# Performance work log

Hardware: AMD Instinct MI355X
Metric: run time of the kernel (lower is better)

## Reference

```python
import jax, jax.numpy as jnp
import numpy as np

# Static config matching init_kwargs / input_specs
IN_CH = 256
PATCH = 64
LAYERS = 4
B, H, W = 4, 256, 256
IC = IN_CH // 4        # SelfAttention inner channels (reduce=4)
C16 = IN_CH // 16      # f_test conv output channels
ALPHA = 0.05


def conv1x1(x, w, b):
    # x: (b,c,h,w), w: (out,c), b: (out,)  == nn.Conv2d(c,out,1)
    return jnp.einsum('bchw,oc->bohw', x, w) + b[None, :, None, None]


def setup_inputs() -> dict:
    key = jax.random.key(0)
    ks = jax.random.split(key, 12)
    s = 0.05
    return {
        'x':  jax.random.normal(ks[0], (B, IN_CH, H, W), jnp.float32),
        'Wq': jax.random.normal(ks[1], (IC, IN_CH), jnp.float32) * s,
        'bq': jax.random.normal(ks[2], (IC,), jnp.float32) * s,
        'Wk': jax.random.normal(ks[3], (IC, IN_CH), jnp.float32) * s,
        'bk': jax.random.normal(ks[4], (IC,), jnp.float32) * s,
        'Wv': jax.random.normal(ks[5], (IC, IN_CH), jnp.float32) * s,
        'bv': jax.random.normal(ks[6], (IC,), jnp.float32) * s,
        'Wr': jax.random.normal(ks[7], (IN_CH, IC), jnp.float32) * s,
        'br': jax.random.normal(ks[8], (IN_CH,), jnp.float32) * s,
        'Wf': jax.random.normal(ks[9], (C16, IN_CH), jnp.float32) * s,
        'bf': jax.random.normal(ks[10], (C16,), jnp.float32) * s,
    }


def reference(x, Wq, bq, Wk, bk, Wv, bv, Wr, br, Wf, bf):
    b, c, h, w = x.shape
    p = PATCH
    nh = h // p
    ic = IC

    # f_test applies the same 1x1 conv to the FULL image every call; its output
    # is identical each time, so precompute the per-(batch,channel) mean/var once.
    # torch uses .detach() -> stop_gradient.
    y2 = jax.lax.stop_gradient(conv1x1(x, Wf, bf))           # (b, C16, h, w)
    m2 = y2.mean(axis=(2, 3))                                 # (b, C16)
    v2 = y2.var(axis=(2, 3))                                  # biased var
    n1 = float(p * p)
    n2 = float(h * w)
    dfw = n1 + n2 - 2.0

    def ftest_decision(patch):
        # Two-group one-way ANOVA (scipy.stats.f_oneway) per (batch, channel).
        y1 = jax.lax.stop_gradient(conv1x1(patch, Wf, bf))    # (b, C16, p, p)
        m1 = y1.mean(axis=(2, 3))
        v1 = y1.var(axis=(2, 3))
        gm = (n1 * m1 + n2 * m2) / (n1 + n2)
        ssb = n1 * (m1 - gm) ** 2 + n2 * (m2 - gm) ** 2       # df_between = 1
        ssw = n1 * v1 + n2 * v2                               # sum sq dev within
        Fst = ssb / (ssw / dfw)
        # p-value = sf of F(1, dfw) = I_{dfw/(dfw+F)}(dfw/2, 1/2)
        pval = jax.scipy.special.betainc(dfw / 2.0, 0.5, dfw / (dfw + Fst))
        counts = jnp.sum(pval < ALPHA)
        return counts * 2 >= m1.size                          # scalar bool

    def attn(patch):
        # SelfAttention.forward: channel-to-channel attention over a patch.
        Q = conv1x1(patch, Wq, bq).reshape(b, ic, p * p)      # (b, ic, pp)
        # NOTE: original does K_pro.view(b, -1, inner_ch) -- a raw reshape,
        # NOT a transpose; we reproduce that exactly.
        K = conv1x1(patch, Wk, bk).reshape(b, p * p, ic)      # (b, pp, ic)
        V = conv1x1(patch, Wv, bv).reshape(b, ic, p * p)
        wts = jax.nn.softmax(jnp.einsum('bim,bmj->bij', Q, K), axis=1)  # (b,ic,ic)
        att = jnp.einsum('bij,bjm->bim', wts, V).reshape(b, ic, p, p)
        return conv1x1(att, Wr, br) + patch

    def run_patch(patch):
        # layer loop with data-dependent early break, expressed via masking
        stopped = jnp.array(False)
        for _ in range(LAYERS):
            stopped = stopped | ftest_decision(patch)  # break BEFORE attention
            patch = jnp.where(stopped, patch, attn(patch))
        return patch

    # Extract all nh*nh patches: (n_patches, b, c, p, p)
    patches = (x.reshape(b, c, nh, p, nh, p)
                .transpose(2, 4, 0, 1, 3, 5)
                .reshape(nh * nh, b, c, p, p))
    out_patches = jax.vmap(run_patch)(patches)

    # Faithful to original bug: x1 = x.clone() happens inside the patch loop,
    # so only the LAST patch's update survives in the returned tensor.
    x1 = x.at[:, :, (nh - 1) * p:, (nh - 1) * p:].set(out_patches[-1])
    return x1
```

## Files before the change

kernel.cpp:

```cpp
#include <hip/hip_runtime.h>

#define FCRIT 3.8415923532

#define OFF_FULL   0u
#define OFF_PATCH  1024u
#define OFF_S      8192u
#define OFF_Y3     1048576u
#define STATS_ZERO_BYTES 270336u

static __device__ __forceinline__ double wred(double v) {
#pragma unroll
  for (int off = 32; off > 0; off >>= 1) v += __shfl_down(v, off, 64);
  return v;
}

static __device__ __forceinline__ bool is_stopped(const double* __restrict__ fullS,
                                                  const double* __restrict__ patchS,
                                                  int upto) {
  const int k = threadIdx.x & 63;
  const double fs = fullS[2 * k], fq = fullS[2 * k + 1];
  const double m2 = fs * (1.0 / 65536.0);
  const double v2 = fq * (1.0 / 65536.0) - m2 * m2;
  bool stopped = false;
  for (int l = 0; l <= upto; ++l) {
    const double* ps = patchS + (size_t)l * 128;
    const double s1 = ps[2 * k], s2 = ps[2 * k + 1];
    const double m1 = s1 * (1.0 / 4096.0);
    const double v1 = s2 * (1.0 / 4096.0) - m1 * m1;
    const double gm = (4096.0 * m1 + 65536.0 * m2) * (1.0 / 69632.0);
    const double d1 = m1 - gm, d2 = m2 - gm;
    const double ssb = 4096.0 * d1 * d1 + 65536.0 * d2 * d2;
    const double ssw = 4096.0 * v1 + 65536.0 * v2;
    const double F = ssb * (69630.0 / ssw);
    const unsigned long long bal = __ballot(F > FCRIT);
    const int cnt = __popcll(bal);
    stopped = stopped || (2 * cnt >= 64);
  }
  return stopped;
}

static __device__ __forceinline__ void fma16(float acc[4][4], float4 w, float4 v) {
  const float wa[4] = {w.x, w.y, w.z, w.w};
  const float va[4] = {v.x, v.y, v.z, v.w};
#pragma unroll
  for (int a = 0; a < 4; ++a)
#pragma unroll
    for (int c = 0; c < 4; ++c) acc[a][c] += wa[a] * va[c];
}

static __device__ __forceinline__ size_t pidx(int b, int c, int y, int x) {
  return (((size_t)b * 256 + c) * 256 + 192 + y) * 256 + 192 + x;
}

__global__ __launch_bounds__(256) void k_main(const float* __restrict__ x,
                                              const float* __restrict__ Wf,
                                              const float* __restrict__ bf,
                                              float* __restrict__ out,
                                              double* __restrict__ fullS,
                                              double* __restrict__ patchS0) {
  __shared__ __align__(16) float WfT2[16 * 257];
  __shared__ __align__(16) float WfT[256 * 16];
  __shared__ double sm[4][16][2];
  __shared__ double sp[4][16][2];
  const int t = threadIdx.x;
  const int bb = blockIdx.x >> 7;
  const int rp = blockIdx.x & 127;

  for (int r = 0; r < 16; ++r) {
    int idx = r * 256 + t;
    WfT2[(idx >> 8) * 257 + (idx & 255)] = Wf[idx];
  }
  __syncthreads();
  for (int r = 0; r < 16; ++r) {
    int idx = r * 256 + t;
    int c = idx >> 4, o = idx & 15;
    WfT[c * 16 + o] = WfT2[o * 257 + c];
  }
  __syncthreads();

  const int r0 = rp * 2 + (t >> 7);
  const int col2 = (t & 127) * 2;
  const size_t base = (size_t)bb * 16777216 + (size_t)r0 * 256 + col2;
  const float* xp = x + base;
  float* op = out + base;
  const bool pStore = (rp >= 96) && ((t & 127) >= 96);

  float y0[16], y1[16];
#pragma unroll
  for (int o = 0; o < 16; ++o) { y0[o] = 0.f; y1[o] = 0.f; }

  for (int cb = 0; cb < 32; ++cb) {
    double v[8];
#pragma unroll
    for (int u = 0; u < 8; ++u)
      v[u] = *reinterpret_cast<const double*>(xp + (size_t)(cb * 8 + u) * 65536);
#pragma unroll
    for (int u = 0; u < 8; ++u) {
      double* dst = reinterpret_cast<double*>(op + (size_t)(cb * 8 + u) * 65536);
      if (pStore) *dst = v[u];
      else __builtin_nontemporal_store(v[u], dst);
      const int c = cb * 8 + u;
      float2 f = *reinterpret_cast<const float2*>(&v[u]);
      const float4* wf = reinterpret_cast<const float4*>(&WfT[c * 16]);
      const float4 w0 = wf[0], w1 = wf[1], w2 = wf[2], w3 = wf[3];
      const float wv[16] = {w0.x, w0.y, w0.z, w0.w, w1.x, w1.y, w1.z, w1.w,
                            w2.x, w2.y, w2.z, w2.w, w3.x, w3.y, w3.z, w3.w};
#pragma unroll
      for (int o = 0; o < 16; ++o) {
        y0[o] += wv[o] * f.x;
        y1[o] += wv[o] * f.y;
      }
    }
  }

  const int w = t >> 6, lane = t & 63;
  const bool pBlock = (rp >= 96);
  const bool pLane = ((t & 127) >= 96);
#pragma unroll 1
  for (int o = 0; o < 16; ++o) {
    const float bo = bf[o];
    const double a0 = (double)(y0[o] + bo), a1 = (double)(y1[o] + bo);
    double s1 = a0 + a1, s2 = a0 * a0 + a1 * a1;
    const double r1 = wred(s1), r2 = wred(s2);
    if (lane == 0) { sm[w][o][0] = r1; sm[w][o][1] = r2; }
    if (pBlock) {
      double p1 = pLane ? s1 : 0.0, p2 = pLane ? s2 : 0.0;
      p1 = wred(p1); p2 = wred(p2);
      if (lane == 0) { sp[w][o][0] = p1; sp[w][o][1] = p2; }
    }
  }
  __syncthreads();
  if (t < 32) {
    const int o = t >> 1, wh = t & 1;
    double s = sm[0][o][wh] + sm[1][o][wh] + sm[2][o][wh] + sm[3][o][wh];
    unsafeAtomicAdd(&fullS[(bb * 16 + o) * 2 + wh], s);
    if (pBlock) {
      double p = sp[0][o][wh] + sp[1][o][wh] + sp[2][o][wh] + sp[3][o][wh];
      unsafeAtomicAdd(&patchS0[(bb * 16 + o) * 2 + wh], p);
    }
  }
}

__global__ __launch_bounds__(256) void k_qkv(const float* __restrict__ out,
                                             const float* __restrict__ Wq, const float* __restrict__ bq,
                                             const float* __restrict__ Wk, const float* __restrict__ bk,
                                             const float* __restrict__ Wv, const float* __restrict__ bv,
                                             float* __restrict__ Y3,
                                             const double* __restrict__ fullS,
                                             const double* __restrict__ patchS, int layer) {
  if (is_stopped(fullS, patchS, layer)) return;
  __shared__ __align__(16) float W3T[64][68];
  __shared__ __align__(16) float X2[64 * 64];
  const int t = threadIdx.x;
  const int blk = blockIdx.x;
  const int qt = blk & 63;
  const int mt = (blk >> 6) % 3;
  const int bb = blk / 192;
  const float* Wm = (mt == 0) ? Wq : (mt == 1) ? Wk : Wv;
  const float* bm = (mt == 0) ? bq : (mt == 1) ? bk : bv;
  const int tq = t & 15, to = t >> 4;
  float acc[4][4] = {};
  for (int kc = 0; kc < 4; ++kc) {
    const int k0 = kc * 64;
    __syncthreads();
    for (int r = 0; r < 16; ++r) {
      int idx = r * 256 + t;
      int ml = idx >> 6, kl = idx & 63;
      W3T[kl][ml] = Wm[ml * 256 + k0 + kl];
    }
    for (int r = 0; r < 16; ++r) {
      int idx = r * 256 + t;
      int kl = idx >> 6, ql = idx & 63;
      X2[kl * 64 + ql] = out[pidx(bb, k0 + kl, qt, ql)];
    }
    __syncthreads();
#pragma unroll 8
    for (int kk = 0; kk < 64; ++kk) {
      const float4 wv = *reinterpret_cast<const float4*>(&W3T[kk][to * 4]);
      const float4 xv = *reinterpret_cast<const float4*>(&X2[kk * 64 + tq * 4]);
      fma16(acc, wv, xv);
    }
  }
#pragma unroll
  for (int a = 0; a < 4; ++a) {
    const int ml = to * 4 + a;
    const float bias = bm[ml];
    float4 res;
    res.x = acc[a][0] + bias;
    res.y = acc[a][1] + bias;
    res.z = acc[a][2] + bias;
    res.w = acc[a][3] + bias;
    *reinterpret_cast<float4*>(&Y3[((size_t)bb * 192 + mt * 64 + ml) * 4096 + qt * 64 + tq * 4]) = res;
  }
}

__global__ __launch_bounds__(256) void k_s(const float* __restrict__ Y3,
                                           float* __restrict__ Sbase,
                                           const double* __restrict__ fullS,
                                           const double* __restrict__ patchS, int layer) {
  if (is_stopped(fullS, patchS, layer)) return;
  __shared__ __align__(16) float QT[64][68];
  __shared__ __align__(16) float K2[64 * 64];
  const int t = threadIdx.x;
  const int mc = blockIdx.x & 63;
  const int bb = blockIdx.x >> 6;
  const int m0 = mc * 64;
  const float* Q = Y3 + (size_t)bb * 192 * 4096;
  const float* Kf = Q + 64 * 4096;
  for (int r = 0; r < 16; ++r) {
    int idx = r * 256 + t;
    int i = idx >> 6, ml = idx & 63;
    QT[ml][i] = Q[(size_t)i * 4096 + m0 + ml];
  }
  for (int r = 0; r < 16; ++r) {
    int idx = r * 256 + t;
    K2[idx] = Kf[(size_t)m0 * 64 + idx];
  }
  __syncthreads();
  const int tj = t & 15, ti = t >> 4;
  float acc[4][4] = {};
#pragma unroll 8
  for (int mm = 0; mm < 64; ++mm) {
    const float4 qv = *reinterpret_cast<const float4*>(&QT[mm][ti * 4]);
    const float4 kv = *reinterpret_cast<const float4*>(&K2[mm * 64 + tj * 4]);
    fma16(acc, qv, kv);
  }
  float* Sl = Sbase + (size_t)layer * 16384 + bb * 4096;
#pragma unroll
  for (int a = 0; a < 4; ++a)
#pragma unroll
    for (int c = 0; c < 4; ++c)
      unsafeAtomicAdd(&Sl[(ti * 4 + a) * 64 + tj * 4 + c], acc[a][c]);
}

__global__ __launch_bounds__(256) void k_awr(const float* __restrict__ Y3,
                                             const float* __restrict__ Sbase,
                                             const float* __restrict__ Wr,
                                             const float* __restrict__ br,
                                             float* __restrict__ out,
                                             const double* __restrict__ fullS,
                                             const double* __restrict__ patchS, int layer) {
  if (is_stopped(fullS, patchS, layer)) return;
  __shared__ __align__(16) float Sw[64 * 68];
  __shared__ __align__(16) float AV[64 * 68];
  __shared__ __align__(16) float WrF[128 * 65];
  const int t = threadIdx.x;
  const int y = blockIdx.x & 63;
  const int oh = (blockIdx.x >> 6) & 1;
  const int bb = blockIdx.x >> 7;

  const float* Vp = Y3 + (size_t)bb * 192 * 4096 + (size_t)128 * 4096 + y * 64;
  for (int r = 0; r < 16; ++r) {
    int idx = r * 256 + t;
    int j = idx >> 6, xx = idx & 63;
    AV[j * 68 + xx] = Vp[(size_t)j * 4096 + xx];
  }
  const float* Sl = Sbase + (size_t)layer * 16384 + bb * 4096;
  for (int r = 0; r < 16; ++r) {
    int idx = r * 256 + t;
    Sw[(idx & 63) * 68 + (idx >> 6)] = Sl[idx];
  }
  for (int r = 0; r < 32; ++r) {
    int idx = r * 256 + t;
    int ol = idx >> 6, i = idx & 63;
    WrF[ol * 65 + i] = Wr[(oh * 128 + ol) * 64 + i];
  }
  __syncthreads();

  if (t < 64) {
    float* colp = &Sw[t * 68];
    float mx = -1e30f;
#pragma unroll
    for (int i = 0; i < 64; ++i) mx = fmaxf(mx, colp[i]);
    float sum = 0.f;
#pragma unroll
    for (int i = 0; i < 64; ++i) {
      float e = __expf(colp[i] - mx);
      colp[i] = e;
      sum += e;
    }
    const float inv = 1.f / sum;
#pragma unroll
    for (int i = 0; i < 64; ++i) colp[i] *= inv;
  }
  __syncthreads();

  {
    const int ti = t >> 4, tx = t & 15;
    float acc[4][4] = {};
#pragma unroll 8
    for (int j = 0; j < 64; ++j) {
      const float4 wv = *reinterpret_cast<const float4*>(&Sw[j * 68 + ti * 4]);
      const float4 vv = *reinterpret_cast<const float4*>(&AV[j * 68 + tx * 4]);
      fma16(acc, wv, vv);
    }
    __syncthreads();
#pragma unroll
    for (int a = 0; a < 4; ++a) {
      float4 res;
      res.x = acc[a][0]; res.y = acc[a][1]; res.z = acc[a][2]; res.w = acc[a][3];
      *reinterpret_cast<float4*>(&AV[(ti * 4 + a) * 68 + tx * 4]) = res;
    }
  }
  __syncthreads();

  const int to = t >> 3, tx8 = t & 7;
  float acc[4][8] = {};
#pragma unroll 4
  for (int i = 0; i < 64; ++i) {
    const float4 a0 = *reinterpret_cast<const float4*>(&AV[i * 68 + tx8 * 8]);
    const float4 a1 = *reinterpret_cast<const float4*>(&AV[i * 68 + tx8 * 8 + 4]);
    const float av[8] = {a0.x, a0.y, a0.z, a0.w, a1.x, a1.y, a1.z, a1.w};
#pragma unroll
    for (int a = 0; a < 4; ++a) {
      const float wv = WrF[(to * 4 + a) * 65 + i];
#pragma unroll
      for (int c = 0; c < 8; ++c) acc[a][c] += wv * av[c];
    }
  }
#pragma unroll
  for (int a = 0; a < 4; ++a) {
    const int o = oh * 128 + to * 4 + a;
    const float bro = br[o];
    float* p = out + pidx(bb, o, y, tx8 * 8);
    float4 p0 = *reinterpret_cast<const float4*>(p);
    float4 p1 = *reinterpret_cast<const float4*>(p + 4);
    p0.x += acc[a][0] + bro; p0.y += acc[a][1] + bro;
    p0.z += acc[a][2] + bro; p0.w += acc[a][3] + bro;
    p1.x += acc[a][4] + bro; p1.y += acc[a][5] + bro;
    p1.z += acc[a][6] + bro; p1.w += acc[a][7] + bro;
    *reinterpret_cast<float4*>(p) = p0;
    *reinterpret_cast<float4*>(p + 4) = p1;
  }
}

__global__ __launch_bounds__(256) void k_ftest(const float* __restrict__ out,
                                               const float* __restrict__ Wf,
                                               const float* __restrict__ bf,
                                               double* __restrict__ patchS,
                                               const double* __restrict__ fullS, int layer) {
  if (is_stopped(fullS, patchS, layer)) return;
  __shared__ __align__(16) float WfT2[16 * 257];
  __shared__ __align__(16) float WfT[256 * 16];
  __shared__ float part[2 * 128 * 17];
  __shared__ double red[16][16][2];
  const int t = threadIdx.x;
  const int bb = blockIdx.x >> 5;
  const int rg = blockIdx.x & 31;

  for (int r = 0; r < 16; ++r) {
    int idx = r * 256 + t;
    WfT2[(idx >> 8) * 257 + (idx & 255)] = Wf[idx];
  }
  __syncthreads();
  for (int r = 0; r < 16; ++r) {
    int idx = r * 256 + t;
    int c = idx >> 4, o = idx & 15;
    WfT[c * 16 + o] = WfT2[o * 257 + c];
  }
  __syncthreads();

  const int h = t >> 7;
  const int px = t & 127;
  const int row = 192 + rg * 2 + (px >> 6);
  const int col = 192 + (px & 63);
  const size_t base = (size_t)bb * 16777216 + (size_t)h * 128 * 65536 + (size_t)row * 256 + col;

  float y[16] = {};
  for (int cb = 0; cb < 16; ++cb) {
    float v[8];
#pragma unroll
    for (int u = 0; u < 8; ++u)
      v[u] = out[base + (size_t)(cb * 8 + u) * 65536];
#pragma unroll
    for (int u = 0; u < 8; ++u) {
      const int c = h * 128 + cb * 8 + u;
      const float4* wf = reinterpret_cast<const float4*>(&WfT[c * 16]);
      const float4 w0 = wf[0], w1 = wf[1], w2 = wf[2], w3 = wf[3];
      const float wv[16] = {w0.x, w0.y, w0.z, w0.w, w1.x, w1.y, w1.z, w1.w,
                            w2.x, w2.y, w2.z, w2.w, w3.x, w3.y, w3.z, w3.w};
#pragma unroll
      for (int o = 0; o < 16; ++o) y[o] += wv[o] * v[u];
    }
  }
#pragma unroll
  for (int o = 0; o < 16; ++o) part[(h * 128 + px) * 17 + o] = y[o];
  __syncthreads();

  const int oo = t & 15, pxg = t >> 4;
  double s1 = 0.0, s2 = 0.0;
  const float bo = bf[oo];
#pragma unroll
  for (int j = 0; j < 8; ++j) {
    const int p = pxg * 8 + j;
    const float yv = part[p * 17 + oo] + part[(128 + p) * 17 + oo] + bo;
    const double v = (double)yv;
    s1 += v;
    s2 += v * v;
  }
  red[oo][pxg][0] = s1;
  red[oo][pxg][1] = s2;
  __syncthreads();
  if (t < 32) {
    const int o = t >> 1, wh = t & 1;
    double s = 0.0;
#pragma unroll
    for (int g = 0; g < 16; ++g) s += red[o][g][wh];
    unsafeAtomicAdd(&patchS[(size_t)(layer + 1) * 128 + (bb * 16 + o) * 2 + wh], s);
  }
}

extern "C" void kernel_launch(void* const* d_in, const int* in_sizes, int n_in,
                              void* d_out, int out_size, void* d_ws, size_t ws_size,
                              hipStream_t stream) {
  const float* x  = (const float*)d_in[0];
  const float* Wq = (const float*)d_in[1];
  const float* bq = (const float*)d_in[2];
  const float* Wk = (const float*)d_in[3];
  const float* bk = (const float*)d_in[4];
  const float* Wv = (const float*)d_in[5];
  const float* bv = (const float*)d_in[6];
  const float* Wr = (const float*)d_in[7];
  const float* br = (const float*)d_in[8];
  const float* Wf = (const float*)d_in[9];
  const float* bf = (const float*)d_in[10];
  float* out = (float*)d_out;
  char* ws = (char*)d_ws;

  double* fullS  = (double*)(ws + OFF_FULL);
  double* patchS = (double*)(ws + OFF_PATCH);
  float* Sb = (float*)(ws + OFF_S);
  float* Y3 = (float*)(ws + OFF_Y3);

  (void)hipMemsetAsync(ws, 0, STATS_ZERO_BYTES, stream);
  k_main<<<512, 256, 0, stream>>>(x, Wf, bf, out, fullS, patchS);
  for (int l = 0; l < 4; ++l) {
    k_qkv<<<768, 256, 0, stream>>>(out, Wq, bq, Wk, bk, Wv, bv, Y3, fullS, patchS, l);
    k_s<<<256, 256, 0, stream>>>(Y3, Sb, fullS, patchS, l);
    k_awr<<<512, 256, 0, stream>>>(Y3, Sb, Wr, br, out, fullS, patchS, l);
    if (l < 3) k_ftest<<<128, 256, 0, stream>>>(out, Wf, bf, patchS, fullS, l);
  }
}
```

Baseline: 260.7 us.

## Fuse pipeline into persistent megakernel with split-bf16 MFMA and grid barriers

Replaces the per-layer launch chain (qkv, S, awr, ftest) with one persistent kernel. 192 blocks stream the full-image copy and statistics while 64 blocks process the patch layers, synchronising through global atomic barriers. Patch matmuls use bf16 MFMA with hi/mid/lo weight and hi/mid activation splits to approximate fp32 accuracy, and a small kernel pre-converts the weights. The aim is to remove launch overhead, overlap the bandwidth-bound copy with patch compute, and use matrix cores. The risks are spin-barrier deadlock or timeout if the blocks are not co-resident, and some loss of precision.

```diff
diff --git a/kernel.cpp b/kernel.cpp
--- a/kernel.cpp
+++ b/kernel.cpp
@@ -1,412 +1,621 @@
 #include <hip/hip_runtime.h>
+
+typedef __attribute__((ext_vector_type(8))) short short8;
+typedef __attribute__((ext_vector_type(8))) unsigned short us8;
+typedef __attribute__((ext_vector_type(4))) unsigned short us4;
+typedef __attribute__((ext_vector_type(4))) float f32x4;
 
 #define FCRIT 3.8415923532
 
 #define OFF_FULL   0u
 #define OFF_PATCH  1024u
-#define OFF_S      8192u
-#define OFF_Y3     1048576u
-#define STATS_ZERO_BYTES 270336u
-
+#define OFF_SBUF   8192u
+#define OFF_BAR    270336u
+#define ZERO_BYTES 270592u
+#define OFF_W3H    (1u<<20)
+#define OFF_WRH    (OFF_W3H + 294912u)
+#define OFF_WFH    (OFF_WRH + 98304u)
+#define OFF_QBT    (4u<<20)
+#define OFF_KB     (8u<<20)
+#define OFF_VBT    (12u<<20)
+#define OFF_XB     (16u<<20)
+#define OFF_PB     (32u<<20)
+
+static __device__ __forceinline__ unsigned short f2bf(float f) {
+  union { float f; unsigned u; } v; v.f = f;
+  unsigned r = v.u + 0x7fffu + ((v.u >> 16) & 1u);
+  return (unsigned short)(r >> 16);
+}
+static __device__ __forceinline__ float bf2f(unsigned short h) {
+  union { unsigned u; float f; } v; v.u = ((unsigned)h) << 16;
+  return v.f;
+}
+static __device__ __forceinline__ void split2(float v, unsigned short& h, unsigned short& m) {
+  h = f2bf(v); float r = v - bf2f(h); m = f2bf(r);
+}
 static __device__ __forceinline__ double wred(double v) {
 #pragma unroll
   for (int off = 32; off > 0; off >>= 1) v += __shfl_down(v, off, 64);
   return v;
 }
-
-static __device__ __forceinline__ bool is_stopped(const double* __restrict__ fullS,
-                                                  const double* __restrict__ patchS,
-                                                  int upto) {
-  const int k = threadIdx.x & 63;
-  const double fs = fullS[2 * k], fq = fullS[2 * k + 1];
-  const double m2 = fs * (1.0 / 65536.0);
-  const double v2 = fq * (1.0 / 65536.0) - m2 * m2;
-  bool stopped = false;
-  for (int l = 0; l <= upto; ++l) {
-    const double* ps = patchS + (size_t)l * 128;
-    const double s1 = ps[2 * k], s2 = ps[2 * k + 1];
-    const double m1 = s1 * (1.0 / 4096.0);
-    const double v1 = s2 * (1.0 / 4096.0) - m1 * m1;
-    const double gm = (4096.0 * m1 + 65536.0 * m2) * (1.0 / 69632.0);
-    const double d1 = m1 - gm, d2 = m2 - gm;
-    const double ssb = 4096.0 * d1 * d1 + 65536.0 * d2 * d2;
-    const double ssw = 4096.0 * v1 + 65536.0 * v2;
-    const double F = ssb * (69630.0 / ssw);
-    const unsigned long long bal = __ballot(F > FCRIT);
-    const int cnt = __popcll(bal);
-    stopped = stopped || (2 * cnt >= 64);
-  }
-  return stopped;
-}
-
-static __device__ __forceinline__ void fma16(float acc[4][4], float4 w, float4 v) {
-  const float wa[4] = {w.x, w.y, w.z, w.w};
-  const float va[4] = {v.x, v.y, v.z, v.w};
-#pragma unroll
-  for (int a = 0; a < 4; ++a)
-#pragma unroll
-    for (int c = 0; c < 4; ++c) acc[a][c] += wa[a] * va[c];
-}
-
-static __device__ __forceinline__ size_t pidx(int b, int c, int y, int x) {
-  return (((size_t)b * 256 + c) * 256 + 192 + y) * 256 + 192 + x;
-}
-
-__global__ __launch_bounds__(256) void k_main(const float* __restrict__ x,
-                                              const float* __restrict__ Wf,
-                                              const float* __restrict__ bf,
-                                              float* __restrict__ out,
-                                              double* __restrict__ fullS,
-                                              double* __restrict__ patchS0) {
-  __shared__ __align__(16) float WfT2[16 * 257];
-  __shared__ __align__(16) float WfT[256 * 16];
-  __shared__ double sm[4][16][2];
-  __shared__ double sp[4][16][2];
-  const int t = threadIdx.x;
-  const int bb = blockIdx.x >> 7;
-  const int rp = blockIdx.x & 127;
-
-  for (int r = 0; r < 16; ++r) {
-    int idx = r * 256 + t;
-    WfT2[(idx >> 8) * 257 + (idx & 255)] = Wf[idx];
+static __device__ __forceinline__ void gbar(unsigned* cnt, unsigned target) {
+  __syncthreads();
+  if (threadIdx.x == 0) {
+    __threadfence();
+    atomicAdd(cnt, 1u);
+    unsigned spins = 0;
+    while (__hip_atomic_load(cnt, __ATOMIC_RELAXED, __HIP_MEMORY_SCOPE_AGENT) < target) {
+      __builtin_amdgcn_s_sleep(2);
+      if (++spins > (1u << 20)) break;
+    }
+    __threadfence();
   }
   __syncthreads();
-  for (int r = 0; r < 16; ++r) {
-    int idx = r * 256 + t;
-    int c = idx >> 4, o = idx & 15;
-    WfT[c * 16 + o] = WfT2[o * 257 + c];
+}
+
+__global__ __launch_bounds__(256) void k_wcvt(const float* __restrict__ Wq,
+                                              const float* __restrict__ Wk,
+                                              const float* __restrict__ Wv,
+                                              const float* __restrict__ Wr,
+                                              const float* __restrict__ Wf,
+                                              char* __restrict__ ws) {
+  unsigned short* W3H = (unsigned short*)(ws + OFF_W3H);
+  unsigned short* WRH = (unsigned short*)(ws + OFF_WRH);
+  unsigned short* WFH = (unsigned short*)(ws + OFF_WFH);
+  for (int i = blockIdx.x * 256 + threadIdx.x; i < 69632; i += gridDim.x * 256) {
+    float v; unsigned short* dst; int stride;
+    if (i < 49152) {
+      const int row = i >> 8, col = i & 255;
+      v = (row < 64) ? Wq[row * 256 + col]
+        : (row < 128) ? Wk[(row - 64) * 256 + col]
+                      : Wv[(row - 128) * 256 + col];
+      dst = W3H + i; stride = 49152;
+    } else if (i < 65536) {
+      v = Wr[i - 49152]; dst = WRH + (i - 49152); stride = 16384;
+    } else {
+      v = Wf[i - 65536]; dst = WFH + (i - 65536); stride = 4096;
+    }
+    const unsigned short h = f2bf(v); const float r1 = v - bf2f(h);
+    const unsigned short m = f2bf(r1); const float r2 = r1 - bf2f(m);
+    dst[0] = h; dst[stride] = m; dst[2 * stride] = f2bf(r2);
   }
-  __syncthreads();
-
-  const int r0 = rp * 2 + (t >> 7);
-  const int col2 = (t & 127) * 2;
-  const size_t base = (size_t)bb * 16777216 + (size_t)r0 * 256 + col2;
-  const float* xp = x + base;
-  float* op = out + base;
-  const bool pStore = (rp >= 96) && ((t & 127) >= 96);
-
-  float y0[16], y1[16];
-#pragma unroll
-  for (int o = 0; o < 16; ++o) { y0[o] = 0.f; y1[o] = 0.f; }
-
-  for (int cb = 0; cb < 32; ++cb) {
-    double v[8];
-#pragma unroll
-    for (int u = 0; u < 8; ++u)
-      v[u] = *reinterpret_cast<const double*>(xp + (size_t)(cb * 8 + u) * 65536);
-#pragma unroll
-    for (int u = 0; u < 8; ++u) {
-      double* dst = reinterpret_cast<double*>(op + (size_t)(cb * 8 + u) * 65536);
-      if (pStore) *dst = v[u];
-      else __builtin_nontemporal_store(v[u], dst);
-      const int c = cb * 8 + u;
-      float2 f = *reinterpret_cast<const float2*>(&v[u]);
-      const float4* wf = reinterpret_cast<const float4*>(&WfT[c * 16]);
-      const float4 w0 = wf[0], w1 = wf[1], w2 = wf[2], w3 = wf[3];
-      const float wv[16] = {w0.x, w0.y, w0.z, w0.w, w1.x, w1.y, w1.z, w1.w,
-                            w2.x, w2.y, w2.z, w2.w, w3.x, w3.y, w3.z, w3.w};
-#pragma unroll
-      for (int o = 0; o < 16; ++o) {
-        y0[o] += wv[o] * f.x;
-        y1[o] += wv[o] * f.y;
-      }
-    }
-  }
-
+}
+
+__global__ __launch_bounds__(256, 1) void k_mega(
+    const float* __restrict__ x, const float* __restrict__ bq,
+    const float* __restrict__ bk, const float* __restrict__ bv,
+    const float* __restrict__ br, const float* __restrict__ bf,
+    const float* __restrict__ Wf, float* __restrict__ out,
+    char* __restrict__ ws) {
+  __shared__ __align__(16) char pool[55296];
+  const int t = threadIdx.x;
+  const int bid = blockIdx.x;
+  double* fullS  = (double*)(ws + OFF_FULL);
+  double* patchS = (double*)(ws + OFF_PATCH);
+  float* Sb = (float*)(ws + OFF_SBUF);
+  unsigned* cntA = (unsigned*)(ws + OFF_BAR);
+  unsigned* cntG = (unsigned*)(ws + OFF_BAR + 128);
+  unsigned short* W3H = (unsigned short*)(ws + OFF_W3H);
+  unsigned short* WRH = (unsigned short*)(ws + OFF_WRH);
+  unsigned short* WFH = (unsigned short*)(ws + OFF_WFH);
+  unsigned short* QBT = (unsigned short*)(ws + OFF_QBT);
+  unsigned short* KB  = (unsigned short*)(ws + OFF_KB);
+  unsigned short* VBT = (unsigned short*)(ws + OFF_VBT);
+  unsigned short* XB  = (unsigned short*)(ws + OFF_XB);
+  float* PB = (float*)(ws + OFF_PB);
   const int w = t >> 6, lane = t & 63;
-  const bool pBlock = (rp >= 96);
-  const bool pLane = ((t & 127) >= 96);
-#pragma unroll 1
-  for (int o = 0; o < 16; ++o) {
-    const float bo = bf[o];
-    const double a0 = (double)(y0[o] + bo), a1 = (double)(y1[o] + bo);
-    double s1 = a0 + a1, s2 = a0 * a0 + a1 * a1;
-    const double r1 = wred(s1), r2 = wred(s2);
-    if (lane == 0) { sm[w][o][0] = r1; sm[w][o][1] = r2; }
-    if (pBlock) {
-      double p1 = pLane ? s1 : 0.0, p2 = pLane ? s2 : 0.0;
-      p1 = wred(p1); p2 = wred(p2);
-      if (lane == 0) { sp[w][o][0] = p1; sp[w][o][1] = p2; }
-    }
-  }
-  __syncthreads();
-  if (t < 32) {
-    const int o = t >> 1, wh = t & 1;
-    double s = sm[0][o][wh] + sm[1][o][wh] + sm[2][o][wh] + sm[3][o][wh];
-    unsafeAtomicAdd(&fullS[(bb * 16 + o) * 2 + wh], s);
-    if (pBlock) {
-      double p = sp[0][o][wh] + sp[1][o][wh] + sp[2][o][wh] + sp[3][o][wh];
-      unsafeAtomicAdd(&patchS0[(bb * 16 + o) * 2 + wh], p);
-    }
-  }
-}
-
-__global__ __launch_bounds__(256) void k_qkv(const float* __restrict__ out,
-                                             const float* __restrict__ Wq, const float* __restrict__ bq,
-                                             const float* __restrict__ Wk, const float* __restrict__ bk,
-                                             const float* __restrict__ Wv, const float* __restrict__ bv,
-                                             float* __restrict__ Y3,
-                                             const double* __restrict__ fullS,
-                                             const double* __restrict__ patchS, int layer) {
-  if (is_stopped(fullS, patchS, layer)) return;
-  __shared__ __align__(16) float W3T[64][68];
-  __shared__ __align__(16) float X2[64 * 64];
-  const int t = threadIdx.x;
-  const int blk = blockIdx.x;
-  const int qt = blk & 63;
-  const int mt = (blk >> 6) % 3;
-  const int bb = blk / 192;
-  const float* Wm = (mt == 0) ? Wq : (mt == 1) ? Wk : Wv;
-  const float* bm = (mt == 0) ? bq : (mt == 1) ? bk : bv;
-  const int tq = t & 15, to = t >> 4;
-  float acc[4][4] = {};
-  for (int kc = 0; kc < 4; ++kc) {
-    const int k0 = kc * 64;
+  const int lo16 = lane & 15, hi4 = lane >> 4;
+
+  if (bid < 192) {
+    float* WfT2 = (float*)pool;
+    float* WfT  = (float*)(pool + 16448);
+    double* sm  = (double*)(pool + 32896);
+    for (int r = 0; r < 16; ++r) {
+      int idx = r * 256 + t;
+      WfT2[(idx >> 8) * 257 + (idx & 255)] = Wf[idx];
+    }
     __syncthreads();
     for (int r = 0; r < 16; ++r) {
       int idx = r * 256 + t;
-      int ml = idx >> 6, kl = idx & 63;
-      W3T[kl][ml] = Wm[ml * 256 + k0 + kl];
-    }
-    for (int r = 0; r < 16; ++r) {
-      int idx = r * 256 + t;
-      int kl = idx >> 6, ql = idx & 63;
-      X2[kl * 64 + ql] = out[pidx(bb, k0 + kl, qt, ql)];
+      int c = idx >> 4, o = idx & 15;
+      WfT[c * 16 + o] = WfT2[o * 257 + c];
     }
     __syncthreads();
-#pragma unroll 8
-    for (int kk = 0; kk < 64; ++kk) {
-      const float4 wv = *reinterpret_cast<const float4*>(&W3T[kk][to * 4]);
-      const float4 xv = *reinterpret_cast<const float4*>(&X2[kk * 64 + tq * 4]);
-      fma16(acc, wv, xv);
+    for (int rp = bid; rp < 512; rp += 192) {
+      const int bb = rp >> 7;
+      const int r0 = (rp & 127) * 2 + (t >> 7);
+      const int col2 = (t & 127) * 2;
+      const size_t base = (size_t)bb * 16777216 + (size_t)r0 * 256 + col2;
+      const float* xp = x + base;
+      float* op = out + base;
+      float y0[16], y1[16];
+#pragma unroll
+      for (int o = 0; o < 16; ++o) { y0[o] = 0.f; y1[o] = 0.f; }
+      for (int cb = 0; cb < 32; ++cb) {
+        double v[8];
+#pragma unroll
+        for (int u = 0; u < 8; ++u)
+          v[u] = *reinterpret_cast<const double*>(xp + (size_t)(cb * 8 + u) * 65536);
+#pragma unroll
+        for (int u = 0; u < 8; ++u) {
+          __builtin_nontemporal_store(v[u], reinterpret_cast<double*>(op + (size_t)(cb * 8 + u) * 65536));
+          const int c = cb * 8 + u;
+          float2 f = *reinterpret_cast<const float2*>(&v[u]);
+          const float4* wf = reinterpret_cast<const float4*>(&WfT[c * 16]);
+          const float4 w0 = wf[0], w1 = wf[1], w2 = wf[2], w3 = wf[3];
+          const float wv[16] = {w0.x, w0.y, w0.z, w0.w, w1.x, w1.y, w1.z, w1.w,
+                                w2.x, w2.y, w2.z, w2.w, w3.x, w3.y, w3.z, w3.w};
+#pragma unroll
+          for (int o = 0; o < 16; ++o) {
+            y0[o] += wv[o] * f.x;
+            y1[o] += wv[o] * f.y;
+          }
+        }
+      }
+#pragma unroll 1
+      for (int o = 0; o < 16; ++o) {
+        const float bo = bf[o];
+        const double a0 = (double)(y0[o] + bo), a1 = (double)(y1[o] + bo);
+        double s1 = a0 + a1, s2 = a0 * a0 + a1 * a1;
+        const double r1 = wred(s1), r2 = wred(s2);
+        if (lane == 0) { sm[(w * 16 + o) * 2] = r1; sm[(w * 16 + o) * 2 + 1] = r2; }
+      }
+      __syncthreads();
+      if (t < 32) {
+        const int o = t >> 1, wh = t & 1;
+        double s = sm[o * 2 + wh] + sm[(16 + o) * 2 + wh] + sm[(32 + o) * 2 + wh] + sm[(48 + o) * 2 + wh];
+        unsafeAtomicAdd(&fullS[(bb * 16 + o) * 2 + wh], s);
+      }
+      __syncthreads();
+    }
+  } else {
+    const int bid2 = bid - 192;
+    const int b = bid2 >> 4;
+    const int q16 = bid2 & 15;
+    unsigned barSeq = 0;
+    for (int layer = 0; layer < 4; ++layer) {
+      const float* Pprev = PB + (size_t)(layer - 1) * 4194304;
+      const int px0 = q16 * 256;
+      {
+        unsigned short* XhL = (unsigned short*)pool;
+        unsigned short* XmL = (unsigned short*)(pool + 20480);
+        const int pxg = px0 + t;
+        f32x4 fa[4];
+#pragma unroll
+        for (int nf = 0; nf < 4; ++nf) fa[nf] = (f32x4)0.f;
+        for (int kc = 0; kc < 8; ++kc) {
+          const int c0 = kc * 32;
+          __syncthreads();
+          float vv[32];
+          if (layer == 0) {
+            const float* xp = x + (size_t)b * 16777216 + (size_t)(192 + (pxg >> 6)) * 256
+                              + (192 + (pxg & 63)) + (size_t)c0 * 65536;
+#pragma unroll
+            for (int u = 0; u < 32; ++u) vv[u] = xp[(size_t)u * 65536];
+          } else {
+            const float* pp = Pprev + ((size_t)b * 4096 + pxg) * 256 + c0;
+#pragma unroll
+            for (int u = 0; u < 8; ++u)
+              *reinterpret_cast<float4*>(&vv[u * 4]) = reinterpret_cast<const float4*>(pp)[u];
+          }
+          unsigned short* xh = XB + ((size_t)b * 4096 + pxg) * 256 + c0;
+#pragma unroll
+          for (int g = 0; g < 4; ++g) {
+            us8 hv, mv;
+#pragma unroll
+            for (int j = 0; j < 8; ++j) {
+              unsigned short h, m; split2(vv[g * 8 + j], h, m);
+              hv[j] = h; mv[j] = m;
+            }
+            *(us8*)&XhL[t * 40 + g * 8] = hv;
+            *(us8*)&XmL[t * 40 + g * 8] = mv;
+            *(us8*)(xh + g * 8) = hv;
+            *(us8*)(xh + 4194304 + g * 8) = mv;
+          }
+          __syncthreads();
+          const short8 ah = *(const short8*)(WFH + lo16 * 256 + c0 + hi4 * 8);
+          const short8 am = *(const short8*)(WFH + 4096 + lo16 * 256 + c0 + hi4 * 8);
+          const short8 al = *(const short8*)(WFH + 8192 + lo16 * 256 + c0 + hi4 * 8);
+#pragma unroll
+          for (int nf = 0; nf < 4; ++nf) {
+            const int pxl = w * 64 + nf * 16 + lo16;
+            const short8 bh = *(const short8*)&XhL[pxl * 40 + hi4 * 8];
+            const short8 bm = *(const short8*)&XmL[pxl * 40 + hi4 * 8];
+            f32x4 c = fa[nf];
+            c = __builtin_amdgcn_mfma_f32_16x16x32_bf16(ah, bh, c, 0, 0, 0);
+            c = __builtin_amdgcn_mfma_f32_16x16x32_bf16(ah, bm, c, 0, 0, 0);
+            c = __builtin_amdgcn_mfma_f32_16x16x32_bf16(am, bh, c, 0, 0, 0);
+            c = __builtin_amdgcn_mfma_f32_16x16x32_bf16(am, bm, c, 0, 0, 0);
+            c = __builtin_amdgcn_mfma_f32_16x16x32_bf16(al, bh, c, 0, 0, 0);
+            fa[nf] = c;
+          }
+        }
+#pragma unroll
+        for (int r = 0; r < 4; ++r) {
+          const int o = hi4 * 4 + r;
+          const float bo = bf[o];
+          double s1 = 0.0, s2 = 0.0;
+#pragma unroll
+          for (int nf = 0; nf < 4; ++nf) {
+            const double v = (double)(fa[nf][r] + bo);
+            s1 += v; s2 += v * v;
+          }
+#pragma unroll
+          for (int msk = 1; msk < 16; msk <<= 1) {
+            s1 += __shfl_xor(s1, msk, 64);
+            s2 += __shfl_xor(s2, msk, 64);
+          }
+          if (lo16 == 0) {
+            unsafeAtomicAdd(&patchS[layer * 128 + (b * 16 + o) * 2], s1);
+            unsafeAtomicAdd(&patchS[layer * 128 + (b * 16 + o) * 2 + 1], s2);
+          }
+        }
+      }
+      gbar(cntA, 64 * (++barSeq));
+      {
+        unsigned short* WhL = (unsigned short*)pool;
+        unsigned short* XhB = (unsigned short*)(pool + 30720);
+        const unsigned short* W3L2 = W3H + 2 * 49152;
+        for (int ph = 0; ph < 2; ++ph) {
+          f32x4 bacc[12][2];
+#pragma unroll
+          for (int mf = 0; mf < 12; ++mf)
+#pragma unroll
+            for (int nf = 0; nf < 2; ++nf) bacc[mf][nf] = (f32x4)0.f;
+          for (int kc = 0; kc < 8; ++kc) {
+            const int c0 = kc * 32;
+            __syncthreads();
+#pragma unroll
+            for (int lev = 0; lev < 2; ++lev) {
+#pragma unroll
+              for (int r = 0; r < 3; ++r) {
+                const int unit = r * 256 + t;
+                const int m = unit >> 2, k8 = (unit & 3) * 8;
+                *(us8*)&WhL[lev * 7680 + m * 40 + k8] =
+                    *(const us8*)(W3H + lev * 49152 + m * 256 + c0 + k8);
+              }
+#pragma unroll
+              for (int r = 0; r < 2; ++r) {
+                const int unit = r * 256 + t;
+                const int px = unit >> 2, k8 = (unit & 3) * 8;
+                *(us8*)&XhB[lev * 5120 + px * 40 + k8] =
+                    *(const us8*)(XB + (size_t)lev * 4194304
+                                  + ((size_t)b * 4096 + px0 + ph * 128 + px) * 256 + c0 + k8);
+              }
+            }
+            __syncthreads();
+            short8 xbh[2], xbm[2];
+#pragma unroll
+            for (int nf = 0; nf < 2; ++nf) {
+              const int pxl = w * 32 + nf * 16 + lo16;
+              xbh[nf] = *(const short8*)&XhB[pxl * 40 + hi4 * 8];
+              xbm[nf] = *(const short8*)&XhB[5120 + pxl * 40 + hi4 * 8];
+            }
+#pragma unroll
+            for (int mf = 0; mf < 12; ++mf) {
+              const int m = mf * 16 + lo16;
+              const short8 wh = *(const short8*)&WhL[m * 40 + hi4 * 8];
+              const short8 wm = *(const short8*)&WhL[7680 + m * 40 + hi4 * 8];
+              const short8 wl = *(const short8*)(W3L2 + m * 256 + c0 + hi4 * 8);
+#pragma unroll
+              for (int nf = 0; nf < 2; ++nf) {
+                f32x4 c = bacc[mf][nf];
+                c = __builtin_amdgcn_mfma_f32_16x16x32_bf16(wh, xbh[nf], c, 0, 0, 0);
+                c = __builtin_amdgcn_mfma_f32_16x16x32_bf16(wh, xbm[nf], c, 0, 0, 0);
+                c = __builtin_amdgcn_mfma_f32_16x16x32_bf16(wm, xbh[nf], c, 0, 0, 0);
+                c = __builtin_amdgcn_mfma_f32_16x16x32_bf16(wm, xbm[nf], c, 0, 0, 0);
+                c = __builtin_amdgcn_mfma_f32_16x16x32_bf16(wl, xbh[nf], c, 0, 0, 0);
+                bacc[mf][nf] = c;
+              }
+            }
+          }
+#pragma unroll
+          for (int mf = 0; mf < 12; ++mf) {
+            const int m0 = mf * 16 + hi4 * 4;
+            const float* bias = (m0 < 64) ? bq + m0 : (m0 < 128) ? bk + (m0 - 64) : bv + (m0 - 128);
+#pragma unroll
+            for (int nf = 0; nf < 2; ++nf) {
+              const int pxg = px0 + ph * 128 + w * 32 + nf * 16 + lo16;
+              us4 hv, mv;
+#pragma unroll
+              for (int r = 0; r < 4; ++r) {
+                unsigned short h, m;
+                split2(bacc[mf][nf][r] + bias[r], h, m);
+                hv[r] = h; mv[r] = m;
+              }
+              if (mf < 4) {
+                const size_t o = ((size_t)b * 4096 + pxg) * 64 + m0;
+                *(us4*)(QBT + o) = hv;
+                *(us4*)(QBT + 1048576 + o) = mv;
+              } else if (mf < 8) {
+#pragma unroll
+                for (int r = 0; r < 4; ++r) {
+                  const size_t o = ((size_t)b * 64 + (m0 - 64 + r)) * 4096 + pxg;
+                  KB[o] = hv[r];
+                  KB[1048576 + o] = mv[r];
+                }
+              } else {
+                const size_t o = ((size_t)b * 4096 + pxg) * 64 + (m0 - 128);
+                *(us4*)(VBT + o) = hv;
+                *(us4*)(VBT + 1048576 + o) = mv;
+              }
+            }
+          }
+        }
+      }
+      gbar(cntA, 64 * (++barSeq));
+      {
+        unsigned short* At = (unsigned short*)pool;
+        unsigned short* Bt = (unsigned short*)(pool + 18432);
+        f32x4 cacc[4];
+#pragma unroll
+        for (int mf = 0; mf < 4; ++mf) cacc[mf] = (f32x4)0.f;
+        for (int mcl = 0; mcl < 4; ++mcl) {
+          const int mc = q16 * 4 + mcl;
+          __syncthreads();
+          {
+            const int r2 = t >> 2, ig = (t & 3) * 16;
+#pragma unroll
+            for (int lev = 0; lev < 2; ++lev) {
+              const size_t qb = (size_t)lev * 1048576 + ((size_t)b * 4096 + mc * 64 + r2) * 64 + ig;
+              const us8 v0 = *(const us8*)(QBT + qb);
+              const us8 v1 = *(const us8*)(QBT + qb + 8);
+#pragma unroll
+              for (int ii = 0; ii < 8; ++ii) {
+                At[lev * 4608 + (ig + ii) * 72 + r2] = v0[ii];
+                At[lev * 4608 + (ig + 8 + ii) * 72 + r2] = v1[ii];
+              }
+            }
+            const int p0 = t * 16;
+            const int jj0 = p0 & 63, rr = p0 >> 6;
+#pragma unroll
+            for (int lev = 0; lev < 2; ++lev) {
+              const size_t kb = (size_t)lev * 1048576 + ((size_t)b * 64 + mc) * 4096 + p0;
+              const us8 v0 = *(const us8*)(KB + kb);
+              const us8 v1 = *(const us8*)(KB + kb + 8);
+#pragma unroll
+              for (int ii = 0; ii < 8; ++ii) {
+                Bt[lev * 4608 + (jj0 + ii) * 72 + rr] = v0[ii];
+                Bt[lev * 4608 + (jj0 + 8 + ii) * 72 + rr] = v1[ii];
+              }
+            }
+          }
+          __syncthreads();
+#pragma unroll
+          for (int kc = 0; kc < 2; ++kc) {
+            const short8 bh = *(const short8*)&Bt[(w * 16 + lo16) * 72 + kc * 32 + hi4 * 8];
+            const short8 bm = *(const short8*)&Bt[4608 + (w * 16 + lo16) * 72 + kc * 32 + hi4 * 8];
+#pragma unroll
+            for (int mf = 0; mf < 4; ++mf) {
+              const short8 qh = *(const short8*)&At[(mf * 16 + lo16) * 72 + kc * 32 + hi4 * 8];
+              const short8 qm = *(const short8*)&At[4608 + (mf * 16 + lo16) * 72 + kc * 32 + hi4 * 8];
+              f32x4 c = cacc[mf];
+              c = __builtin_amdgcn_mfma_f32_16x16x32_bf16(qh, bh, c, 0, 0, 0);
+              c = __builtin_amdgcn_mfma_f32_16x16x32_bf16(qh, bm, c, 0, 0, 0);
+              c = __builtin_amdgcn_mfma_f32_16x16x32_bf16(qm, bh, c, 0, 0, 0);
+              c = __builtin_amdgcn_mfma_f32_16x16x32_bf16(qm, bm, c, 0, 0, 0);
+              cacc[mf] = c;
+            }
+          }
+        }
+        float* Sl = Sb + ((size_t)layer * 4 + b) * 4096;
+#pragma unroll
+        for (int mf = 0; mf < 4; ++mf)
+#pragma unroll
+          for (int r = 0; r < 4; ++r)
+            unsafeAtomicAdd(&Sl[(mf * 16 + hi4 * 4 + r) * 64 + w * 16 + lo16], cacc[mf][r]);
+      }
+      gbar(cntA, 64 * (++barSeq));
+      {
+        unsigned short* wtsL = (unsigned short*)pool;
+        unsigned short* AbT  = (unsigned short*)(pool + 18432);
+        float* Sf = (float*)(pool + 18432);
+        const float* Sl = Sb + ((size_t)layer * 4 + b) * 4096;
+        {
+          const int i2 = t >> 2, jg = (t & 3) * 16;
+#pragma unroll
+          for (int u = 0; u < 4; ++u) {
+            const float4 v = *(const float4*)(Sl + i2 * 64 + jg + u * 4);
+            Sf[(jg + u * 4 + 0) * 68 + i2] = v.x;
+            Sf[(jg + u * 4 + 1) * 68 + i2] = v.y;
+            Sf[(jg + u * 4 + 2) * 68 + i2] = v.z;
+            Sf[(jg + u * 4 + 3) * 68 + i2] = v.w;
+          }
+        }
+        __syncthreads();
+        if (t < 64) {
+          float* rowp = &Sf[t * 68];
+          float mx = -1e30f;
+#pragma unroll
+          for (int i = 0; i < 64; ++i) mx = fmaxf(mx, rowp[i]);
+          float sum = 0.f;
+#pragma unroll
+          for (int i = 0; i < 64; ++i) {
+            const float e = __expf(rowp[i] - mx);
+            rowp[i] = e; sum += e;
+          }
+          const float inv = 1.f / sum;
+#pragma unroll
+          for (int i = 0; i < 64; ++i) rowp[i] *= inv;
+        }
+        __syncthreads();
+        {
+          const int i2 = t >> 2, jg = (t & 3) * 16;
+#pragma unroll
+          for (int u = 0; u < 2; ++u) {
+            us8 hv, mv;
+#pragma unroll
+            for (int jj = 0; jj < 8; ++jj) {
+              unsigned short h, m;
+              split2(Sf[(jg + u * 8 + jj) * 68 + i2], h, m);
+              hv[jj] = h; mv[jj] = m;
+            }
+            *(us8*)&wtsL[i2 * 72 + jg + u * 8] = hv;
+            *(us8*)&wtsL[4608 + i2 * 72 + jg + u * 8] = mv;
+          }
+        }
+        __syncthreads();
+        float* PBl = PB + (size_t)layer * 4194304;
+        for (int ph = 0; ph < 2; ++ph) {
+          f32x4 a1[4][2];
+#pragma unroll
+          for (int mf = 0; mf < 4; ++mf)
+#pragma unroll
+            for (int nf = 0; nf < 2; ++nf) a1[mf][nf] = (f32x4)0.f;
+#pragma unroll
+          for (int kc = 0; kc < 2; ++kc) {
+            short8 vh[2], vm[2];
+#pragma unroll
+            for (int nf = 0; nf < 2; ++nf) {
+              const int pxg = px0 + ph * 128 + w * 32 + nf * 16 + lo16;
+              const size_t vb = ((size_t)b * 4096 + pxg) * 64 + kc * 32 + hi4 * 8;
+              vh[nf] = *(const short8*)(VBT + vb);
+              vm[nf] = *(const short8*)(VBT + 1048576 + vb);
+            }
+#pragma unroll
+            for (int mf = 0; mf < 4; ++mf) {
+              const short8 wh = *(const short8*)&wtsL[(mf * 16 + lo16) * 72 + kc * 32 + hi4 * 8];
+              const short8 wm = *(const short8*)&wtsL[4608 + (mf * 16 + lo16) * 72 + kc * 32 + hi4 * 8];
+#pragma unroll
+              for (int nf = 0; nf < 2; ++nf) {
+                f32x4 c = a1[mf][nf];
+                c = __builtin_amdgcn_mfma_f32_16x16x32_bf16(wh, vh[nf], c, 0, 0, 0);
+                c = __builtin_amdgcn_mfma_f32_16x16x32_bf16(wh, vm[nf], c, 0, 0, 0);
+                c = __builtin_amdgcn_mfma_f32_16x16x32_bf16(wm, vh[nf], c, 0, 0, 0);
+                c = __builtin_amdgcn_mfma_f32_16x16x32_bf16(wm, vm[nf], c, 0, 0, 0);
+                a1[mf][nf] = c;
+              }
+            }
+          }
+#pragma unroll
+          for (int mf = 0; mf < 4; ++mf)
+#pragma unroll
+            for (int nf = 0; nf < 2; ++nf) {
+              const int pxl = w * 32 + nf * 16 + lo16;
+              const int i0 = mf * 16 + hi4 * 4;
+              us4 hv, mv;
+#pragma unroll
+              for (int r = 0; r < 4; ++r) {
+                unsigned short h, m;
+                split2(a1[mf][nf][r], h, m);
+                hv[r] = h; mv[r] = m;
+              }
+              *(us4*)&AbT[pxl * 72 + i0] = hv;
+              *(us4*)&AbT[9216 + pxl * 72 + i0] = mv;
+            }
+          __syncthreads();
+          f32x4 a2[16][2];
+#pragma unroll
+          for (int mf = 0; mf < 16; ++mf)
+#pragma unroll
+            for (int nf = 0; nf < 2; ++nf) a2[mf][nf] = (f32x4)0.f;
+#pragma unroll
+          for (int kc = 0; kc < 2; ++kc) {
+            short8 abh[2], abm[2];
+#pragma unroll
+            for (int nf = 0; nf < 2; ++nf) {
+              const int pxl = w * 32 + nf * 16 + lo16;
+              abh[nf] = *(const short8*)&AbT[pxl * 72 + kc * 32 + hi4 * 8];
+              abm[nf] = *(const short8*)&AbT[9216 + pxl * 72 + kc * 32 + hi4 * 8];
+            }
+#pragma unroll
+            for (int mf = 0; mf < 16; ++mf) {
+              const int o = mf * 16 + lo16;
+              const short8 rh = *(const short8*)(WRH + o * 64 + kc * 32 + hi4 * 8);
+              const short8 rm = *(const short8*)(WRH + 16384 + o * 64 + kc * 32 + hi4 * 8);
+              const short8 rl = *(const short8*)(WRH + 32768 + o * 64 + kc * 32 + hi4 * 8);
+#pragma unroll
+              for (int nf = 0; nf < 2; ++nf) {
+                f32x4 c = a2[mf][nf];
+                c = __builtin_amdgcn_mfma_f32_16x16x32_bf16(rh, abh[nf], c, 0, 0, 0);
+                c = __builtin_amdgcn_mfma_f32_16x16x32_bf16(rh, abm[nf], c, 0, 0, 0);
+                c = __builtin_amdgcn_mfma_f32_16x16x32_bf16(rm, abh[nf], c, 0, 0, 0);
+                c = __builtin_amdgcn_mfma_f32_16x16x32_bf16(rm, abm[nf], c, 0, 0, 0);
+                c = __builtin_amdgcn_mfma_f32_16x16x32_bf16(rl, abh[nf], c, 0, 0, 0);
+                a2[mf][nf] = c;
+              }
+            }
+          }
+#pragma unroll
+          for (int mf = 0; mf < 16; ++mf) {
+#pragma unroll
+            for (int nf = 0; nf < 2; ++nf) {
+              const int pxg = px0 + ph * 128 + w * 32 + nf * 16 + lo16;
+              const int o0 = mf * 16 + hi4 * 4;
+              float4 res;
+              if (layer == 0) {
+                const float* xp = x + (size_t)b * 16777216 + (size_t)(192 + (pxg >> 6)) * 256
+                                  + (192 + (pxg & 63));
+#pragma unroll
+                for (int r = 0; r < 4; ++r)
+                  (&res.x)[r] = a2[mf][nf][r] + br[o0 + r] + xp[(size_t)(o0 + r) * 65536];
+              } else {
+                const float4 pv = *(const float4*)(Pprev + ((size_t)b * 4096 + pxg) * 256 + o0);
+#pragma unroll
+                for (int r = 0; r < 4; ++r)
+                  (&res.x)[r] = a2[mf][nf][r] + br[o0 + r] + (&pv.x)[r];
+              }
+              *(float4*)(PBl + ((size_t)b * 4096 + pxg) * 256 + o0) = res;
+            }
+          }
+          __syncthreads();
+        }
+      }
+      gbar(cntA, 64 * (++barSeq));
     }
   }
-#pragma unroll
-  for (int a = 0; a < 4; ++a) {
-    const int ml = to * 4 + a;
-    const float bias = bm[ml];
-    float4 res;
-    res.x = acc[a][0] + bias;
-    res.y = acc[a][1] + bias;
-    res.z = acc[a][2] + bias;
-    res.w = acc[a][3] + bias;
-    *reinterpret_cast<float4*>(&Y3[((size_t)bb * 192 + mt * 64 + ml) * 4096 + qt * 64 + tq * 4]) = res;
+
+  gbar(cntG, 256);
+  int jsel = 4;
+  {
+    const int k = t & 63;
+    const double fs = fullS[2 * k], fq = fullS[2 * k + 1];
+    const double m2 = fs * (1.0 / 65536.0);
+    const double v2 = fq * (1.0 / 65536.0) - m2 * m2;
+#pragma unroll
+    for (int l = 0; l < 4; ++l) {
+      const double* ps = patchS + l * 128;
+      const double s1 = ps[2 * k], s2 = ps[2 * k + 1];
+      const double m1 = s1 * (1.0 / 4096.0);
+      const double v1 = s2 * (1.0 / 4096.0) - m1 * m1;
+      const double gm = (4096.0 * m1 + 65536.0 * m2) * (1.0 / 69632.0);
+      const double d1 = m1 - gm, d2 = m2 - gm;
+      const double ssb = 4096.0 * d1 * d1 + 65536.0 * d2 * d2;
+      const double ssw = 4096.0 * v1 + 65536.0 * v2;
+      const double F = ssb * (69630.0 / ssw);
+      const unsigned long long bal = __ballot(F > FCRIT);
+      if (2 * __popcll(bal) >= 64 && jsel == 4) jsel = l;
+    }
   }
-}
-
-__global__ __launch_bounds__(256) void k_s(const float* __restrict__ Y3,
-                                           float* __restrict__ Sbase,
-                                           const double* __restrict__ fullS,
-                                           const double* __restrict__ patchS, int layer) {
-  if (is_stopped(fullS, patchS, layer)) return;
-  __shared__ __align__(16) float QT[64][68];
-  __shared__ __align__(16) float K2[64 * 64];
-  const int t = threadIdx.x;
-  const int mc = blockIdx.x & 63;
-  const int bb = blockIdx.x >> 6;
-  const int m0 = mc * 64;
-  const float* Q = Y3 + (size_t)bb * 192 * 4096;
-  const float* Kf = Q + 64 * 4096;
-  for (int r = 0; r < 16; ++r) {
-    int idx = r * 256 + t;
-    int i = idx >> 6, ml = idx & 63;
-    QT[ml][i] = Q[(size_t)i * 4096 + m0 + ml];
-  }
-  for (int r = 0; r < 16; ++r) {
-    int idx = r * 256 + t;
-    K2[idx] = Kf[(size_t)m0 * 64 + idx];
-  }
-  __syncthreads();
-  const int tj = t & 15, ti = t >> 4;
-  float acc[4][4] = {};
-#pragma unroll 8
-  for (int mm = 0; mm < 64; ++mm) {
-    const float4 qv = *reinterpret_cast<const float4*>(&QT[mm][ti * 4]);
-    const float4 kv = *reinterpret_cast<const float4*>(&K2[mm * 64 + tj * 4]);
-    fma16(acc, qv, kv);
-  }
-  float* Sl = Sbase + (size_t)layer * 16384 + bb * 4096;
-#pragma unroll
-  for (int a = 0; a < 4; ++a)
-#pragma unroll
-    for (int c = 0; c < 4; ++c)
-      unsafeAtomicAdd(&Sl[(ti * 4 + a) * 64 + tj * 4 + c], acc[a][c]);
-}
-
-__global__ __launch_bounds__(256) void k_awr(const float* __restrict__ Y3,
-                                             const float* __restrict__ Sbase,
-                                             const float* __restrict__ Wr,
-                                             const float* __restrict__ br,
-                                             float* __restrict__ out,
-                                             const double* __restrict__ fullS,
-                                             const double* __restrict__ patchS, int layer) {
-  if (is_stopped(fullS, patchS, layer)) return;
-  __shared__ __align__(16) float Sw[64 * 68];
-  __shared__ __align__(16) float AV[64 * 68];
-  __shared__ __align__(16) float WrF[128 * 65];
-  const int t = threadIdx.x;
-  const int y = blockIdx.x & 63;
-  const int oh = (blockIdx.x >> 6) & 1;
-  const int bb = blockIdx.x >> 7;
-
-  const float* Vp = Y3 + (size_t)bb * 192 * 4096 + (size_t)128 * 4096 + y * 64;
-  for (int r = 0; r < 16; ++r) {
-    int idx = r * 256 + t;
-    int j = idx >> 6, xx = idx & 63;
-    AV[j * 68 + xx] = Vp[(size_t)j * 4096 + xx];
-  }
-  const float* Sl = Sbase + (size_t)layer * 16384 + bb * 4096;
-  for (int r = 0; r < 16; ++r) {
-    int idx = r * 256 + t;
-    Sw[(idx & 63) * 68 + (idx >> 6)] = Sl[idx];
-  }
-  for (int r = 0; r < 32; ++r) {
-    int idx = r * 256 + t;
-    int ol = idx >> 6, i = idx & 63;
-    WrF[ol * 65 + i] = Wr[(oh * 128 + ol) * 64 + i];
-  }
-  __syncthreads();
-
-  if (t < 64) {
-    float* colp = &Sw[t * 68];
-    float mx = -1e30f;
-#pragma unroll
-    for (int i = 0; i < 64; ++i) mx = fmaxf(mx, colp[i]);
-    float sum = 0.f;
-#pragma unroll
-    for (int i = 0; i < 64; ++i) {
-      float e = __expf(colp[i] - mx);
-      colp[i] = e;
-      sum += e;
-    }
-    const float inv = 1.f / sum;
-#pragma unroll
-    for (int i = 0; i < 64; ++i) colp[i] *= inv;
-  }
-  __syncthreads();
-
-  {
-    const int ti = t >> 4, tx = t & 15;
-    float acc[4][4] = {};
-#pragma unroll 8
-    for (int j = 0; j < 64; ++j) {
-      const float4 wv = *reinterpret_cast<const float4*>(&Sw[j * 68 + ti * 4]);
-      const float4 vv = *reinterpret_cast<const float4*>(&AV[j * 68 + tx * 4]);
-      fma16(acc, wv, vv);
-    }
-    __syncthreads();
-#pragma unroll
-    for (int a = 0; a < 4; ++a) {
-      float4 res;
-      res.x = acc[a][0]; res.y = acc[a][1]; res.z = acc[a][2]; res.w = acc[a][3];
-      *reinterpret_cast<float4*>(&AV[(ti * 4 + a) * 68 + tx * 4]) = res;
-    }
-  }
-  __syncthreads();
-
-  const int to = t >> 3, tx8 = t & 7;
-  float acc[4][8] = {};
-#pragma unroll 4
-  for (int i = 0; i < 64; ++i) {
-    const float4 a0 = *reinterpret_cast<const float4*>(&AV[i * 68 + tx8 * 8]);
-    const float4 a1 = *reinterpret_cast<const float4*>(&AV[i * 68 + tx8 * 8 + 4]);
-    const float av[8] = {a0.x, a0.y, a0.z, a0.w, a1.x, a1.y, a1.z, a1.w};
-#pragma unroll
-    for (int a = 0; a < 4; ++a) {
-      const float wv = WrF[(to * 4 + a) * 65 + i];
-#pragma unroll
-      for (int c = 0; c < 8; ++c) acc[a][c] += wv * av[c];
-    }
-  }
-#pragma unroll
-  for (int a = 0; a < 4; ++a) {
-    const int o = oh * 128 + to * 4 + a;
-    const float bro = br[o];
-    float* p = out + pidx(bb, o, y, tx8 * 8);
-    float4 p0 = *reinterpret_cast<const float4*>(p);
-    float4 p1 = *reinterpret_cast<const float4*>(p + 4);
-    p0.x += acc[a][0] + bro; p0.y += acc[a][1] + bro;
-    p0.z += acc[a][2] + bro; p0.w += acc[a][3] + bro;
-    p1.x += acc[a][4] + bro; p1.y += acc[a][5] + bro;
-    p1.z += acc[a][6] + bro; p1.w += acc[a][7] + bro;
-    *reinterpret_cast<float4*>(p) = p0;
-    *reinterpret_cast<float4*>(p + 4) = p1;
-  }
-}
-
-__global__ __launch_bounds__(256) void k_ftest(const float* __restrict__ out,
-                                               const float* __restrict__ Wf,
-                                               const float* __restrict__ bf,
-                                               double* __restrict__ patchS,
-                                               const double* __restrict__ fullS, int layer) {
-  if (is_stopped(fullS, patchS, layer)) return;
-  __shared__ __align__(16) float WfT2[16 * 257];
-  __shared__ __align__(16) float WfT[256 * 16];
-  __shared__ float part[2 * 128 * 17];
-  __shared__ double red[16][16][2];
-  const int t = threadIdx.x;
-  const int bb = blockIdx.x >> 5;
-  const int rg = blockIdx.x & 31;
-
-  for (int r = 0; r < 16; ++r) {
-    int idx = r * 256 + t;
-    WfT2[(idx >> 8) * 257 + (idx & 255)] = Wf[idx];
-  }
-  __syncthreads();
-  for (int r = 0; r < 16; ++r) {
-    int idx = r * 256 + t;
-    int c = idx >> 4, o = idx & 15;
-    WfT[c * 16 + o] = WfT2[o * 257 + c];
-  }
-  __syncthreads();
-
-  const int h = t >> 7;
-  const int px = t & 127;
-  const int row = 192 + rg * 2 + (px >> 6);
-  const int col = 192 + (px & 63);
-  const size_t base = (size_t)bb * 16777216 + (size_t)h * 128 * 65536 + (size_t)row * 256 + col;
-
-  float y[16] = {};
-  for (int cb = 0; cb < 16; ++cb) {
-    float v[8];
-#pragma unroll
-    for (int u = 0; u < 8; ++u)
-      v[u] = out[base + (size_t)(cb * 8 + u) * 65536];
-#pragma unroll
-    for (int u = 0; u < 8; ++u) {
-      const int c = h * 128 + cb * 8 + u;
-      const float4* wf = reinterpret_cast<const float4*>(&WfT[c * 16]);
-      const float4 w0 = wf[0], w1 = wf[1], w2 = wf[2], w3 = wf[3];
-      const float wv[16] = {w0.x, w0.y, w0.z, w0.w, w1.x, w1.y, w1.z, w1.w,
-                            w2.x, w2.y, w2.z, w2.w, w3.x, w3.y, w3.z, w3.w};
-#pragma unroll
-      for (int o = 0; o < 16; ++o) y[o] += wv[o] * v[u];
-    }
-  }
-#pragma unroll
-  for (int o = 0; o < 16; ++o) part[(h * 128 + px) * 17 + o] = y[o];
-  __syncthreads();
-
-  const int oo = t & 15, pxg = t >> 4;
-  double s1 = 0.0, s2 = 0.0;
-  const float bo = bf[oo];
-#pragma unroll
-  for (int j = 0; j < 8; ++j) {
-    const int p = pxg * 8 + j;
-    const float yv = part[p * 17 + oo] + part[(128 + p) * 17 + oo] + bo;
-    const double v = (double)yv;
-    s1 += v;
-    s2 += v * v;
-  }
-  red[oo][pxg][0] = s1;
-  red[oo][pxg][1] = s2;
-  __syncthreads();
-  if (t < 32) {
-    const int o = t >> 1, wh = t & 1;
-    double s = 0.0;
-#pragma unroll
-    for (int g = 0; g < 16; ++g) s += red[o][g][wh];
-    unsafeAtomicAdd(&patchS[(size_t)(layer + 1) * 128 + (bb * 16 + o) * 2 + wh], s);
+  if (jsel > 0) {
+    const float* src = PB + (size_t)(jsel - 1) * 4194304;
+    const int b2 = bid >> 6, y = bid & 63;
+    float* T = (float*)pool;
+    for (int oc = 0; oc < 4; ++oc) {
+      __syncthreads();
+      {
+        const int pxl = t >> 2, og = (t & 3) * 16;
+#pragma unroll
+        for (int u = 0; u < 4; ++u) {
+          const float4 v = *(const float4*)(src + ((size_t)b2 * 4096 + y * 64 + pxl) * 256
+                                            + oc * 64 + og + u * 4);
+          *(float4*)&T[pxl * 68 + og + u * 4] = v;
+        }
+      }
+      __syncthreads();
+      {
+        const int ol = t & 63, pg = t >> 6;
+        float* op = out + (size_t)b2 * 16777216 + (size_t)(oc * 64 + ol) * 65536
+                    + (size_t)(192 + y) * 256 + 192 + pg * 16;
+#pragma unroll
+        for (int u4 = 0; u4 < 4; ++u4) {
+          float4 v;
+#pragma unroll
+          for (int r = 0; r < 4; ++r) (&v.x)[r] = T[(pg * 16 + u4 * 4 + r) * 68 + ol];
+          *(float4*)(op + u4 * 4) = v;
+        }
+      }
+    }
   }
 }
 
@@ -427,17 +636,7 @@
   float* out = (float*)d_out;
   char* ws = (char*)d_ws;
 
-  double* fullS  = (double*)(ws + OFF_FULL);
-  double* patchS = (double*)(ws + OFF_PATCH);
-  float* Sb = (float*)(ws + OFF_S);
-  float* Y3 = (float*)(ws + OFF_Y3);
-
-  (void)hipMemsetAsync(ws, 0, STATS_ZERO_BYTES, stream);
-  k_main<<<512, 256, 0, stream>>>(x, Wf, bf, out, fullS, patchS);
-  for (int l = 0; l < 4; ++l) {
-    k_qkv<<<768, 256, 0, stream>>>(out, Wq, bq, Wk, bk, Wv, bv, Y3, fullS, patchS, l);
-    k_s<<<256, 256, 0, stream>>>(Y3, Sb, fullS, patchS, l);
-    k_awr<<<512, 256, 0, stream>>>(Y3, Sb, Wr, br, out, fullS, patchS, l);
-    if (l < 3) k_ftest<<<128, 256, 0, stream>>>(out, Wf, bf, patchS, fullS, l);
-  }
-}
+  (void)hipMemsetAsync(ws, 0, ZERO_BYTES, stream);
+  k_wcvt<<<96, 256, 0, stream>>>(Wq, Wk, Wv, Wr, Wf, ws);
+  k_mega<<<256, 256, 0, stream>>>(x, bq, bk, bv, br, bf, Wf, out, ws);
+}
```

Result: slower. 957.5 us (+267.3%).
